# Kernel optimization log

Measured on AMD Instinct MI355X. Metric: run time of the kernel, lower is better.

The kernel has to match this reference:

```python
import jax, jax.numpy as jnp
import numpy as np

N_DOF = 7
WIDTH = 1024
BATCH = 8192
EPS = 1e-5
LSIZE = N_DOF * (N_DOF + 1) // 2   # diag (n) + strictly-lower ((n^2-n)/2)


def _tri_idx(n):
    # order matches LowTri: offset -i chunks, within-chunk j -> entry (j+i, j)
    r, c = [], []
    for i in range(n):
        for j in range(n - i):
            r.append(j + i)
            c.append(j)
    return np.array(r, np.int32), np.array(c, np.int32)

_R, _C = _tri_idx(N_DOF)


def setup_inputs() -> dict:
    key = jax.random.key(0)
    ks = jax.random.split(key, 9)

    def glorot(k, shape):
        std = (2.0 / (shape[0] + shape[1])) ** 0.5
        return (jax.random.normal(k, shape, jnp.float32) * std).astype(jnp.float32)

    lower = LSIZE - N_DOF
    b0 = 0.1
    return {
        "state": jax.random.normal(ks[0], (BATCH, N_DOF), jnp.float32),
        "velocity": jax.random.normal(ks[1], (BATCH, N_DOF), jnp.float32),
        "acceleration": jax.random.normal(ks[2], (BATCH, N_DOF), jnp.float32),
        "W_in": glorot(ks[3], (N_DOF, WIDTH)), "b_in": jnp.full((WIDTH,), b0, jnp.float32),
        "W_h": glorot(ks[4], (WIDTH, WIDTH)), "b_h": jnp.full((WIDTH,), b0, jnp.float32),
        "W_g": glorot(ks[5], (WIDTH, 1)), "b_g": jnp.full((1,), b0, jnp.float32),
        "W_ld": glorot(ks[6], (WIDTH, N_DOF)), "b_ld": jnp.full((N_DOF,), b0, jnp.float32),
        "W_lo": glorot(ks[7], (WIDTH, lower)), "b_lo": jnp.full((lower,), b0, jnp.float32),
    }


def _layer(x, der, W, b, act):
    # a: [B, out]; der: [B, in, n_dof] -> [B, out, n_dof]
    a = x @ W + b
    if act == "relu":
        y = jax.nn.relu(a)
        gp = (a > 0).astype(a.dtype)
    else:  # linear
        y = a
        gp = jnp.ones_like(a)
    # diag(g'(a)) @ W^T @ prev_der  ==  g'(a)[:, :, None] * (W^T @ prev_der)
    new_der = gp[:, :, None] * jnp.einsum("io,bid->bod", W, der)
    return y, new_der


def _forward(state, velocity, acceleration,
             W_in, b_in, W_h, b_h, W_g, b_g, W_ld, b_ld, W_lo, b_lo):
    B = state.shape[0]
    eye = jnp.broadcast_to(jnp.eye(N_DOF, dtype=state.dtype), (B, N_DOF, N_DOF))

    y1, d1 = _layer(state, eye, W_in, b_in, "relu")
    y2, d2 = _layer(y1, d1, W_h, b_h, "relu")
    y3, d3 = _layer(y2, d2, W_h, b_h, "relu")   # original reuses hidden_layer1 twice

    V, derV = _layer(y3, d3, W_g, b_g, "linear")       # derV: [B, 1, n_dof]
    l_diag, der_ld = _layer(y3, d3, W_ld, b_ld, "relu")
    l_low, der_lo = _layer(y3, d3, W_lo, b_lo, "linear")

    l = jnp.concatenate([l_diag, l_low], axis=1)          # [B, LSIZE]
    der_l = jnp.concatenate([der_ld, der_lo], axis=1)     # [B, LSIZE, n_dof]

    def lowtri(v):   # [B, LSIZE] -> [B, n, n]
        return jnp.zeros((B, N_DOF, N_DOF), v.dtype).at[:, _R, _C].set(v)

    def lowtri3d(v):  # [B, n_dof, LSIZE] -> [B, n_dof, n, n]
        return jnp.zeros((B, N_DOF, N_DOF, N_DOF), v.dtype).at[:, :, _R, _C].set(v)

    L = lowtri(l)
    LT = jnp.swapaxes(L, 1, 2)
    M = L @ LT + EPS * jnp.eye(N_DOF, dtype=L.dtype)

    dldt = jnp.einsum("bld,bd->bl", der_l, velocity)
    dLdt = lowtri(dldt)
    dMdt = L @ jnp.swapaxes(dLdt, 1, 2) + dLdt @ LT

    dLdq = lowtri3d(jnp.swapaxes(der_l, 1, 2))            # [B, n_dof, n, n]
    dMdq = dLdq @ LT[:, None] + L[:, None] @ jnp.swapaxes(dLdq, 2, 3)

    dMdt_dq = jnp.einsum("bij,bj->bi", dMdt, velocity)
    quad_dq = jnp.einsum("bi,bkij,bj->bk", velocity, dMdq, velocity)
    C = dMdt_dq - 0.5 * quad_dq
    G = derV[:, 0, :]                                      # squeeze [B,1,n_dof]
    Mddq = jnp.einsum("bij,bj->bi", M, acceleration)
    tau_pred = Mddq + C + G
    return tau_pred, M, C, G


def reference(state, velocity, acceleration,
              W_in, b_in, W_h, b_h, W_g, b_g, W_ld, b_ld, W_lo, b_lo):
    return _forward(state, velocity, acceleration,
                    W_in, b_in, W_h, b_h, W_g, b_g, W_ld, b_ld, W_lo, b_lo)
```

## Files before the change

### kernel.cpp

```cpp
#include <hip/hip_runtime.h>
#include <hip/hip_bf16.h>
#include <hip/hip_fp16.h>

#define WIDTH 1024
#define BATCH 8192

typedef __attribute__((ext_vector_type(8))) short short8;
typedef __attribute__((ext_vector_type(8))) _Float16 half8;
typedef __attribute__((ext_vector_type(4))) float floatx4;

typedef __attribute__((address_space(1))) void gvoid;
typedef __attribute__((address_space(3))) void lvoid;

__device__ __forceinline__ void async_copy16(const void* g, void* l) {
    __builtin_amdgcn_global_load_lds((gvoid*)g, (lvoid*)l, 16, 0, 0);
}

__device__ __forceinline__ void split_store(float v, __hip_bfloat16* hi, __hip_bfloat16* lo, long idx) {
    __hip_bfloat16 h = __float2bfloat16(v);
    hi[idx] = h;
    lo[idx] = __float2bfloat16(v - __bfloat162float(h));
}

__device__ __forceinline__ floatx4 mfma16(short8 a, short8 b, floatx4 c) {
    return __builtin_amdgcn_mfma_f32_16x16x32_f16(
        __builtin_bit_cast(half8, a), __builtin_bit_cast(half8, b), c, 0, 0, 0);
}
__device__ __forceinline__ floatx4 mfmabf(short8 a, short8 b, floatx4 c) {
    return __builtin_amdgcn_mfma_f32_16x16x32_bf16(a, b, c, 0, 0, 0);
}

template<int N> __device__ __forceinline__ void waitv() {
    if constexpr (N == 0)      asm volatile("s_waitcnt vmcnt(0)" ::: "memory");
    else if constexpr (N == 4) asm volatile("s_waitcnt vmcnt(4)" ::: "memory");
    else if constexpr (N == 6) asm volatile("s_waitcnt vmcnt(6)" ::: "memory");
    else if constexpr (N == 8) asm volatile("s_waitcnt vmcnt(8)" ::: "memory");
}

__device__ __forceinline__ int swz_col(int s) {
    return ((s & 3) ^ ((s >> 3) & 3)) << 3;
}

__device__ __forceinline__ void xcd_map(int idx, int nm, int& bm, int& bn) {
    if ((nm & 7) == 0) {
        bm = (idx & 7) | ((idx >> 5) << 3);
        bn = (idx >> 3) & 3;
    } else {
        bm = idx >> 2;
        bn = idx & 3;
    }
}

__global__ __launch_bounds__(256) void transpose_k(
    const float* __restrict__ W,
    __hip_bfloat16* __restrict__ Wthb, __hip_bfloat16* __restrict__ Wtlb,
    __half* __restrict__ Wtf)
{
    __shared__ float t[32][33];
    const int tx = threadIdx.x & 31, ty = threadIdx.x >> 5;
    const int bx = blockIdx.x << 5, by = blockIdx.y << 5;
#pragma unroll
    for (int r = 0; r < 32; r += 8)
        t[ty + r][tx] = W[(long)(by + ty + r) * WIDTH + bx + tx];
    __syncthreads();
#pragma unroll
    for (int r = 0; r < 32; r += 8) {
        const float v = t[tx][ty + r];
        const long idx = (long)(bx + ty + r) * WIDTH + by + tx;
        split_store(v, Wthb, Wtlb, idx);
        Wtf[idx] = __float2half(v);
    }
}

__global__ __launch_bounds__(256) void buildwcat_k(
    const float* __restrict__ W_ld, const float* __restrict__ W_lo,
    const float* __restrict__ W_g,
    __hip_bfloat16* __restrict__ Wchb, __hip_bfloat16* __restrict__ Wclb,
    __half* __restrict__ Wcf)
{
    const int idx = blockIdx.x * 256 + threadIdx.x;
    const int n = idx >> 10, k = idx & 1023;
    float v = 0.f;
    if (n < 7)       v = W_ld[k * 7 + n];
    else if (n < 28) v = W_lo[k * 21 + (n - 7)];
    else if (n == 28) v = W_g[k];
    split_store(v, Wchb, Wclb, idx);
    Wcf[idx] = __float2half(v);
}

__global__ __launch_bounds__(256) void prep_k(
    const float* __restrict__ state,
    const float* __restrict__ W_in,
    const float* __restrict__ b_in,
    __hip_bfloat16* __restrict__ Y1h, __hip_bfloat16* __restrict__ Y1l,
    __half* __restrict__ D1f)
{
    const int b = blockIdx.x;
    const int j0 = threadIdx.x * 4;
    float s[7];
#pragma unroll
    for (int d = 0; d < 7; ++d) s[d] = state[b * 7 + d];
    float a[4];
#pragma unroll
    for (int q = 0; q < 4; ++q) a[q] = b_in[j0 + q];
    float w[7][4];
#pragma unroll
    for (int d = 0; d < 7; ++d)
#pragma unroll
        for (int q = 0; q < 4; ++q) {
            w[d][q] = W_in[d * WIDTH + j0 + q];
            a[q] += s[d] * w[d][q];
        }
    bool gp[4];
#pragma unroll
    for (int q = 0; q < 4; ++q) {
        gp[q] = a[q] > 0.f;
        split_store(gp[q] ? a[q] : 0.f, Y1h, Y1l, (long)b * WIDTH + j0 + q);
    }
    union { unsigned long long u64; unsigned short h[4]; } pk;
#pragma unroll
    for (int d = 0; d < 7; ++d) {
#pragma unroll
        for (int q = 0; q < 4; ++q) {
            __half v = __float2half(gp[q] ? w[d][q] : 0.f);
            pk.h[q] = *reinterpret_cast<unsigned short*>(&v);
        }
        *reinterpret_cast<unsigned long long*>(&D1f[((long)b * 7 + d) * WIDTH + j0]) = pk.u64;
    }
}

__device__ __forceinline__ void st128(const short* src, short* region, int tid, int kbase) {
    async_copy16(src + (long)(tid >> 2) * WIDTH + kbase + swz_col(tid),
                 region + ((tid & 0x1C0) << 3));
}
__device__ __forceinline__ void st256(const short* src, short* region, int tid, int kbase) {
#pragma unroll
    for (int j = 0; j < 2; ++j) {
        const int idx = tid + (j << 9);
        async_copy16(src + (long)(idx >> 2) * WIDTH + kbase + swz_col(idx),
                     region + (((tid & 0x1C0) + (j << 9)) << 3));
    }
}


__device__ __forceinline__ void y_stage(
    short* SM, const short* pAh, const short* pAl,
    const short* pBh, const short* pBl, int c, int tid)
{
    short* buf = SM + (c % 3) * 24576;
    const int kb = c * 32;
    st128(pAh, buf,         tid, kb);
    st256(pBh, buf + 8192,  tid, kb);
    st128(pAl, buf + 4096,  tid, kb);
    st256(pBl, buf + 16384, tid, kb);
}

__device__ __forceinline__ void y_reads(
    const short* SM, int c, int wm, int wn, int r, int kqs,
    short8 (&ah)[4], short8 (&al)[4], short8 (&bh)[4], short8 (&bl)[4])
{
    const short* buf = SM + (c % 3) * 24576;
#pragma unroll
    for (int i = 0; i < 4; ++i) {
        ah[i] = *reinterpret_cast<const short8*>(&buf[(wm * 64 + i * 16 + r) * 32 + kqs]);
        al[i] = *reinterpret_cast<const short8*>(&buf[4096 + (wm * 64 + i * 16 + r) * 32 + kqs]);
    }
#pragma unroll
    for (int j = 0; j < 4; ++j) {
        bh[j] = *reinterpret_cast<const short8*>(&buf[8192 + (wn * 64 + j * 16 + r) * 32 + kqs]);
        bl[j] = *reinterpret_cast<const short8*>(&buf[16384 + (wn * 64 + j * 16 + r) * 32 + kqs]);
    }
}

__device__ __forceinline__ void y8_gemm_body(
    short* SM,
    int bm, int bn, int tid,
    const __hip_bfloat16* Ah_, const __hip_bfloat16* Al_,
    const __hip_bfloat16* Bh_, const __hip_bfloat16* Bl_,
    const float* bias,
    __hip_bfloat16* outh, __hip_bfloat16* outl)
{
    const int lane = tid & 63, wv = tid >> 6;
    const int wm = wv >> 2, wn = wv & 3;
    const int r = lane & 15, r4 = (lane >> 4) << 2;
    const int kqs = (((lane >> 4) ^ ((r >> 1) & 3)) << 3);
    const short* pAh = (const short*)Ah_ + (long)bm * 128 * WIDTH;
    const short* pAl = (const short*)Al_ + (long)bm * 128 * WIDTH;
    const short* pBh = (const short*)Bh_ + (long)bn * 256 * WIDTH;
    const short* pBl = (const short*)Bl_ + (long)bn * 256 * WIDTH;

    floatx4 acc[4][4] = {};
    short8 ahA[4], alA[4], bhA[4], blA[4];
    short8 ahB[4], alB[4], bhB[4], blB[4];

    y_stage(SM, pAh, pAl, pBh, pBl, 0, tid);
    y_stage(SM, pAh, pAl, pBh, pBl, 1, tid);
    y_stage(SM, pAh, pAl, pBh, pBl, 2, tid);
    waitv<6>();
    __builtin_amdgcn_s_barrier();
    y_reads(SM, 0, wm, wn, r, kqs, ahA, alA, bhA, blA);

    auto chunk = [&](short8 (&cah)[4], short8 (&cal)[4], short8 (&cbh)[4], short8 (&cbl)[4],
                     short8 (&nah)[4], short8 (&nal)[4], short8 (&nbh)[4], short8 (&nbl)[4],
                     int c) {
        __builtin_amdgcn_s_barrier();
        if (c + 3 < 32) y_stage(SM, pAh, pAl, pBh, pBl, c + 3, tid);
        if (c + 1 < 32) y_reads(SM, c + 1, wm, wn, r, kqs, nah, nal, nbh, nbl);
        __builtin_amdgcn_s_setprio(1);
#pragma unroll
        for (int i = 0; i < 4; ++i)
#pragma unroll
            for (int j = 0; j < 4; ++j)
                acc[i][j] = mfmabf(cah[i], cbh[j], acc[i][j]);
#pragma unroll
        for (int i = 0; i < 4; ++i)
#pragma unroll
            for (int j = 0; j < 4; ++j)
                acc[i][j] = mfmabf(cal[i], cbh[j], acc[i][j]);
#pragma unroll
        for (int i = 0; i < 4; ++i)
#pragma unroll
            for (int j = 0; j < 4; ++j)
                acc[i][j] = mfmabf(cah[i], cbl[j], acc[i][j]);
        __builtin_amdgcn_s_setprio(0);
        if (c <= 28) waitv<6>();
        else if (c == 29) waitv<0>();
    };

    for (int t2 = 0; t2 < 16; ++t2) {
        chunk(ahA, alA, bhA, blA, ahB, alB, bhB, blB, 2 * t2);
        chunk(ahB, alB, bhB, blB, ahA, alA, bhA, blA, 2 * t2 + 1);
    }

#pragma unroll
    for (int i = 0; i < 4; ++i)
#pragma unroll
        for (int j = 0; j < 4; ++j) {
            const int col = bn * 256 + wn * 64 + j * 16 + r;
#pragma unroll
            for (int rr = 0; rr < 4; ++rr) {
                const int row = bm * 128 + wm * 64 + i * 16 + r4 + rr;
                float v = acc[i][j][rr] + bias[col];
                v = v > 0.f ? v : 0.f;
                split_store(v, outh, outl, (long)row * WIDTH + col);
            }
        }
}

__global__ __launch_bounds__(512, 2) void gemm_y8(
    const __hip_bfloat16* __restrict__ Ah, const __hip_bfloat16* __restrict__ Al,
    const __hip_bfloat16* __restrict__ Bh, const __hip_bfloat16* __restrict__ Bl,
    const float* __restrict__ bias,
    __hip_bfloat16* __restrict__ outh, __hip_bfloat16* __restrict__ outl,
    int ny)
{
    __shared__ __align__(16) short SM[73728];
    int bm, bn;
    xcd_map(blockIdx.x, ny, bm, bn);
    y8_gemm_body(SM, bm, bn, threadIdx.x, Ah, Al, Bh, Bl, bias, outh, outl);
}


__device__ __forceinline__ void stage_chunk_d2(
    short* SMbase, const short* __restrict__ A, const short* __restrict__ B,
    int tau, int creg, int tid)
{
    const short* src = (creg & 1) ? B : A;
    const int kbase = (tau << 6) + ((creg >> 1) << 5);
    short* region = SMbase + ((tau & 1) << 15) + (creg << 13);
    const int wvb = tid & 0x1C0;
#pragma unroll
    for (int j = 0; j < 2; ++j) {
        const int idx = tid + (j << 9);
        async_copy16(src + (long)(idx >> 2) * WIDTH + kbase + swz_col(idx),
                     region + ((long)(wvb + (j << 9)) << 3));
    }
}

__device__ __forceinline__ void d_stage(
    short* SM, const short* A, const short* B, int c, int tid)
{
    stage_chunk_d2(SM, A, B, c >> 1, (c & 1) << 1, tid);
    stage_chunk_d2(SM, A, B, c >> 1, ((c & 1) << 1) | 1, tid);
}

__device__ __forceinline__ void d_reads(
    const short* SM, int c, int wm, int wn, int r, int kqs,
    short8 (&af)[8], short8 (&bf)[4])
{
    const short* Ab = SM + (((c >> 1) & 1) << 15) + ((c & 1) << 14);
    const short* Bb = Ab + 8192;
#pragma unroll
    for (int i = 0; i < 8; ++i)
        af[i] = *reinterpret_cast<const short8*>(&Ab[(wm * 128 + i * 16 + r) * 32 + kqs]);
#pragma unroll
    for (int j = 0; j < 4; ++j)
        bf[j] = *reinterpret_cast<const short8*>(&Bb[(wn * 64 + j * 16 + r) * 32 + kqs]);
}

__device__ __forceinline__ void d_gemm_256(
    short* SM, const short* Abase, const short* Bbase, int tid,
    int wm, int wn, int r, int kqs, floatx4 (&acc)[8][4])
{
    short8 afA[8], bfA[4], afB[8], bfB[4];

    d_stage(SM, Abase, Bbase, 0, tid);
    d_stage(SM, Abase, Bbase, 1, tid);
    d_stage(SM, Abase, Bbase, 2, tid);
    d_stage(SM, Abase, Bbase, 3, tid);
    waitv<8>();
    __builtin_amdgcn_s_barrier();
    d_reads(SM, 0, wm, wn, r, kqs, afA, bfA);

    auto chunk = [&](short8 (&caf)[8], short8 (&cbf)[4],
                     short8 (&naf)[8], short8 (&nbf)[4], int c) {
        __builtin_amdgcn_s_barrier();
        if (c + 4 < 32) d_stage(SM, Abase, Bbase, c + 4, tid);
        if (c + 1 < 32) d_reads(SM, c + 1, wm, wn, r, kqs, naf, nbf);
        __builtin_amdgcn_s_setprio(1);
#pragma unroll
        for (int i = 0; i < 8; ++i)
#pragma unroll
            for (int j = 0; j < 4; ++j)
                acc[i][j] = mfma16(caf[i], cbf[j], acc[i][j]);
        __builtin_amdgcn_s_setprio(0);
        if (c <= 27) waitv<8>();
        else if (c == 28) waitv<4>();
        else if (c == 29) waitv<0>();
    };

    for (int t2 = 0; t2 < 16; ++t2) {
        chunk(afA, bfA, afB, bfB, 2 * t2);
        chunk(afB, bfB, afA, bfA, 2 * t2 + 1);
    }
}

__global__ __launch_bounds__(512, 2) void d2y3_8p(
    const __half* __restrict__ D1,
    const __half* __restrict__ Wtf,
    const __hip_bfloat16* __restrict__ Wthb, const __hip_bfloat16* __restrict__ Wtlb,
    const __hip_bfloat16* __restrict__ Y2h, const __hip_bfloat16* __restrict__ Y2l,
    const float* __restrict__ bias,
    __half* __restrict__ D2out,
    __hip_bfloat16* __restrict__ Y3h, __hip_bfloat16* __restrict__ Y3l,
    int ny128, int nd2)
{
    __shared__ __align__(16) short SM[73728];
    const int tid = threadIdx.x;

    if ((int)blockIdx.x < ny128 * 4) {
        int bm, bn;
        xcd_map(blockIdx.x, ny128, bm, bn);
        y8_gemm_body(SM, bm, bn, tid, Y2h, Y2l, Wthb, Wtlb, bias, Y3h, Y3l);
        return;
    }

    const int lane = tid & 63, wv = tid >> 6;
    const int wm = wv >> 2, wn = wv & 3;
    const int r = lane & 15, r4 = (lane >> 4) << 2;
    const int kqs = (((lane >> 4) ^ ((r >> 1) & 3)) << 3);

    int bm, bn;
    xcd_map(blockIdx.x - ny128 * 4, nd2, bm, bn);

    floatx4 acc[8][4] = {};
    d_gemm_256(SM, (const short*)D1 + (long)bm * 256 * WIDTH,
               (const short*)Wtf + (long)bn * 256 * WIDTH, tid, wm, wn, r, kqs, acc);

#pragma unroll
    for (int i = 0; i < 8; ++i)
#pragma unroll
        for (int j = 0; j < 4; ++j) {
            const int col = bn * 256 + wn * 64 + j * 16 + r;
#pragma unroll
            for (int rr = 0; rr < 4; ++rr) {
                const int row = bm * 256 + wm * 128 + i * 16 + r4 + rr;
                float v = acc[i][j][rr];
                const unsigned brow = (unsigned)row / 7u;
                if (!(__bfloat162float(Y2h[(long)brow * WIDTH + col]) > 0.f)) v = 0.f;
                D2out[(long)row * WIDTH + col] = __float2half(v);
            }
        }
}

__device__ __forceinline__ void heady_half(
    short* SMh, int bm, int tl,
    const __hip_bfloat16* __restrict__ Y3h, const __hip_bfloat16* __restrict__ Y3l,
    const __hip_bfloat16* __restrict__ Wch, const __hip_bfloat16* __restrict__ Wcl,
    float* __restrict__ PY)
{
    short* Ash = SMh;          short* Asl = SMh + 4096;
    short* Bsh = SMh + 8192;   short* Bsl = SMh + 9216;
    const int lane = tl & 63;
    const int wv = tl >> 6;
    const int r = lane & 15, r4 = (lane >> 4) << 2;
    const int kqs = (((lane >> 4) ^ ((r >> 1) & 3)) << 3);
    const int srow = tl >> 2, scol = (tl & 3) << 3;
    const int swc = (((tl & 3) ^ ((srow >> 1) & 3)) << 3);
    const long half = 64l * WIDTH;
    const short* pAh = (const short*)Y3h + (long)(bm * 128 + srow) * WIDTH + swc;
    const short* pAl = (const short*)Y3l + (long)(bm * 128 + srow) * WIDTH + swc;
    const long boff = (long)srow * WIDTH + scol;
    const short* pBh = (const short*)Wch;  const short* pBl = (const short*)Wcl;

    floatx4 acc[2][2] = {};
    for (int kt = 0; kt < WIDTH; kt += 32) {
        short8 gbh, gbl;
        if (tl < 128) {
            gbh = *reinterpret_cast<const short8*>(pBh + boff + kt);
            gbl = *reinterpret_cast<const short8*>(pBl + boff + kt);
        }
        __syncthreads();
        async_copy16(pAh + kt,        Ash + wv * 512);
        async_copy16(pAh + half + kt, Ash + 2048 + wv * 512);
        async_copy16(pAl + kt,        Asl + wv * 512);
        async_copy16(pAl + half + kt, Asl + 2048 + wv * 512);
        if (tl < 128) {
            *reinterpret_cast<short8*>(&Bsh[srow * 32 + swc]) = gbh;
            *reinterpret_cast<short8*>(&Bsl[srow * 32 + swc]) = gbl;
        }
        __syncthreads();
        short8 afh[2], afl[2], bfh[2], bfl[2];
#pragma unroll
        for (int i = 0; i < 2; ++i) {
            const int ar = (wv * 32 + i * 16 + r) * 32 + kqs;
            afh[i] = *reinterpret_cast<const short8*>(&Ash[ar]);
            afl[i] = *reinterpret_cast<const short8*>(&Asl[ar]);
        }
#pragma unroll
        for (int j = 0; j < 2; ++j) {
            const int br = (j * 16 + r) * 32 + kqs;
            bfh[j] = *reinterpret_cast<const short8*>(&Bsh[br]);
            bfl[j] = *reinterpret_cast<const short8*>(&Bsl[br]);
        }
#pragma unroll
        for (int i = 0; i < 2; ++i)
#pragma unroll
            for (int j = 0; j < 2; ++j) {
                acc[i][j] = mfmabf(afh[i], bfh[j], acc[i][j]);
                acc[i][j] = mfmabf(afh[i], bfl[j], acc[i][j]);
                acc[i][j] = mfmabf(afl[i], bfh[j], acc[i][j]);
            }
    }
#pragma unroll
    for (int i = 0; i < 2; ++i)
#pragma unroll
        for (int j = 0; j < 2; ++j)
#pragma unroll
            for (int rr = 0; rr < 4; ++rr) {
                const int row = bm * 128 + wv * 32 + i * 16 + r4 + rr;
                PY[(long)row * 32 + j * 16 + r] = acc[i][j][rr];
            }
}

__global__ __launch_bounds__(512, 2) void d3pd_8p(
    const __half* __restrict__ D2,
    const __half* __restrict__ Wtf,
    const __hip_bfloat16* __restrict__ Y3h, const __hip_bfloat16* __restrict__ Y3l,
    const __half* __restrict__ Wcf,
    const __hip_bfloat16* __restrict__ Wchb, const __hip_bfloat16* __restrict__ Wclb,
    float* __restrict__ PDpart, float* __restrict__ PY,
    int nd2, int Mrows)
{
    __shared__ __align__(16) short SM[65536];
    const int tid = threadIdx.x;

    if ((int)blockIdx.x >= nd2 * 4) {
        const int hd = (blockIdx.x - nd2 * 4) * 2 + (tid >> 8);
        heady_half(SM + (tid >> 8) * 10240, hd, tid & 255, Y3h, Y3l, Wchb, Wclb, PY);
        return;
    }

    const int lane = tid & 63, wv = tid >> 6;
    const int wm = wv >> 2, wn = wv & 3;
    const int r = lane & 15, kq = (lane >> 4) << 3, r4 = (lane >> 4) << 2;
    const int kqs = (((lane >> 4) ^ ((r >> 1) & 3)) << 3);
    int bm, bn;
    xcd_map(blockIdx.x, nd2, bm, bn);

    floatx4 acc[8][4] = {};
    d_gemm_256(SM, (const short*)D2 + (long)bm * 256 * WIDTH,
               (const short*)Wtf + (long)bn * 256 * WIDTH, tid, wm, wn, r, kqs, acc);

    short* T   = SM;
    short* WcH = SM + 34816;

    floatx4 accp[2][2] = {};
#pragma unroll
    for (int h = 0; h < 2; ++h) {
        __syncthreads();
        if ((wn >> 1) == h) {
#pragma unroll
            for (int i = 0; i < 8; ++i)
#pragma unroll
                for (int j = 0; j < 4; ++j) {
                    const int ct = (wn & 1) * 64 + j * 16 + r;
                    const int colg = bn * 256 + h * 128 + ct;
#pragma unroll
                    for (int rr = 0; rr < 4; ++rr) {
                        const int rowl = wm * 128 + i * 16 + r4 + rr;
                        const int rowg = bm * 256 + rowl;
                        float v = acc[i][j][rr];
                        const unsigned brow = (unsigned)rowg / 7u;
                        if (!(__bfloat162float(Y3h[(long)brow * WIDTH + colg]) > 0.f)) v = 0.f;
                        __half hb = __float2half(v);
                        T[rowl * 136 + ct] = *reinterpret_cast<short*>(&hb);
                    }
                }
        }
        {
            const int n = tid >> 4, k8 = (tid & 15) * 8;
            const short* wh = (const short*)Wcf;
            *reinterpret_cast<short8*>(&WcH[n * 136 + k8]) =
                *reinterpret_cast<const short8*>(wh + (long)n * WIDTH + bn * 256 + h * 128 + k8);
        }
        __syncthreads();
#pragma unroll
        for (int kk = 0; kk < 128; kk += 32) {
            short8 af2[2], bh8[2];
#pragma unroll
            for (int i = 0; i < 2; ++i)
                af2[i] = *reinterpret_cast<const short8*>(&T[(wv * 32 + i * 16 + r) * 136 + kk + kq]);
#pragma unroll
            for (int j = 0; j < 2; ++j)
                bh8[j] = *reinterpret_cast<const short8*>(&WcH[(j * 16 + r) * 136 + kk + kq]);
#pragma unroll
            for (int i = 0; i < 2; ++i)
#pragma unroll
                for (int j = 0; j < 2; ++j)
                    accp[i][j] = mfma16(af2[i], bh8[j], accp[i][j]);
        }
    }
#pragma unroll
    for (int i = 0; i < 2; ++i)
#pragma unroll
        for (int j = 0; j < 2; ++j)
#pragma unroll
            for (int rr = 0; rr < 4; ++rr) {
                const int rowg = bm * 256 + wv * 32 + i * 16 + r4 + rr;
                PDpart[((long)bn * Mrows + rowg) * 32 + j * 16 + r] = accp[i][j][rr];
            }
}

__device__ __forceinline__ int midx(int rr, int cc) {
    const int i = rr - cc;
    return i * 7 - (i * (i - 1)) / 2 + cc;
}

__global__ __launch_bounds__(64) void finalize_k(
    const float* __restrict__ PY,
    const float* __restrict__ PDpart,
    const float* __restrict__ vel_g,
    const float* __restrict__ acc_g,
    const float* __restrict__ b_ld,
    const float* __restrict__ b_lo,
    float* __restrict__ out,
    int b0, int Mrows)
{
    __shared__ float lval[28];
    __shared__ int gpv[7];
    __shared__ float derl[29 * 7];
    __shared__ float Lm[49], Mm[49], dLt[49], uu[49];
    __shared__ float wvv[7], pv[7], Cv[7], Gv[7], tauv[7], vl[7], ac[7];

    const int bl = blockIdx.x, tid = threadIdx.x;
    const int b = b0 + bl;
    if (tid < 28) {
        float s = PY[(long)bl * 32 + tid];
        if (tid < 7) {
            s += b_ld[tid];
            gpv[tid] = s > 0.f;
            lval[tid] = s > 0.f ? s : 0.f;
        } else {
            lval[tid] = s + b_lo[tid - 7];
        }
    }
    if (tid >= 28 && tid < 35) {
        vl[tid - 28] = vel_g[b * 7 + tid - 28];
        ac[tid - 28] = acc_g[b * 7 + tid - 28];
    }
    __syncthreads();
    for (int idx = tid; idx < 203; idx += 64) {
        const int m = idx / 7, d = idx % 7;
        float v = 0.f;
#pragma unroll
        for (int p = 0; p < 4; ++p)
            v += PDpart[((long)p * Mrows + bl * 7 + d) * 32 + m];
        if (m < 7 && !gpv[m]) v = 0.f;
        derl[m * 7 + d] = v;
    }
    __syncthreads();
    if (tid < 49) {
        const int rr = tid / 7, cc = tid % 7;
        Lm[tid] = (rr >= cc) ? lval[midx(rr, cc)] : 0.f;
    }
    __syncthreads();
    if (tid < 49) {
        const int rr = tid / 7, cc = tid % 7;
        float s = 0.f;
        for (int k = 0; k < 7; ++k) s += Lm[rr * 7 + k] * Lm[cc * 7 + k];
        if (rr == cc) s += 1e-5f;
        Mm[tid] = s;
        float t = 0.f;
        if (rr >= cc) {
            const int m = midx(rr, cc);
            for (int d = 0; d < 7; ++d) t += derl[m * 7 + d] * vl[d];
        }
        dLt[tid] = t;
        float u = 0.f;
        for (int r2 = cc; r2 < 7; ++r2) u += vl[r2] * derl[midx(r2, cc) * 7 + rr];
        uu[tid] = u;
    } else if (tid >= 49 && tid < 56) {
        const int j = tid - 49;
        float s = 0.f;
        for (int r2 = 0; r2 < 7; ++r2) s += Lm[r2 * 7 + j] * vl[r2];
        wvv[j] = s;
    }
    __syncthreads();
    if (tid < 7) {
        float s = 0.f;
        for (int r2 = 0; r2 < 7; ++r2) s += dLt[r2 * 7 + tid] * vl[r2];
        pv[tid] = s;
    }
    __syncthreads();
    if (tid < 7) {
        float s = 0.f, q = 0.f, md = 0.f;
        for (int c = 0; c < 7; ++c) {
            s += Lm[tid * 7 + c] * pv[c] + dLt[tid * 7 + c] * wvv[c];
            q += uu[tid * 7 + c] * wvv[c];
            md += Mm[tid * 7 + c] * ac[c];
        }
        Cv[tid] = s - q;
        Gv[tid] = derl[28 * 7 + tid];
        tauv[tid] = md + Cv[tid] + Gv[tid];
    }
    __syncthreads();
    if (tid < 49) out[57344 + (long)b * 49 + tid] = Mm[tid];
    if (tid < 7) {
        out[(long)b * 7 + tid] = tauv[tid];
        out[458752 + (long)b * 7 + tid] = Cv[tid];
        out[516096 + (long)b * 7 + tid] = Gv[tid];
    }
}

extern "C" void kernel_launch(void* const* d_in, const int* in_sizes, int n_in,
                              void* d_out, int out_size, void* d_ws, size_t ws_size,
                              hipStream_t stream)
{
    const float* state = (const float*)d_in[0];
    const float* vel   = (const float*)d_in[1];
    const float* accel = (const float*)d_in[2];
    const float* W_in  = (const float*)d_in[3];
    const float* b_in  = (const float*)d_in[4];
    const float* W_h   = (const float*)d_in[5];
    const float* b_h   = (const float*)d_in[6];
    const float* W_g   = (const float*)d_in[7];
    const float* W_ld  = (const float*)d_in[9];
    const float* b_ld  = (const float*)d_in[10];
    const float* W_lo  = (const float*)d_in[11];
    const float* b_lo  = (const float*)d_in[12];
    float* outp = (float*)d_out;

    char* ws = (char*)d_ws;
    __hip_bfloat16* Wthb = (__hip_bfloat16*)ws; ws += (size_t)WIDTH * WIDTH * 2;
    __hip_bfloat16* Wtlb = (__hip_bfloat16*)ws; ws += (size_t)WIDTH * WIDTH * 2;
    __half*         Wtf  = (__half*)ws;         ws += (size_t)WIDTH * WIDTH * 2;
    __hip_bfloat16* Wchb = (__hip_bfloat16*)ws; ws += 32 * WIDTH * 2;
    __hip_bfloat16* Wclb = (__hip_bfloat16*)ws; ws += 32 * WIDTH * 2;
    __half*         Wcf  = (__half*)ws;         ws += 32 * WIDTH * 2;
    const size_t fixed = (size_t)(ws - (char*)d_ws);

    int CH = 256;
    for (int cand = 8192; cand >= 256; cand >>= 1) {
        size_t need = fixed + (size_t)cand * 36992;
        if (need <= ws_size) { CH = cand; break; }
    }
    const int NCH = BATCH / CH;

    const size_t YB = (size_t)CH * WIDTH * 2;
    const size_t DB = (size_t)CH * 7 * WIDTH * 2;
    __hip_bfloat16* Yah = (__hip_bfloat16*)ws; ws += YB;
    __hip_bfloat16* Yal = (__hip_bfloat16*)ws; ws += YB;
    __hip_bfloat16* Ybh = (__hip_bfloat16*)ws; ws += YB;
    __hip_bfloat16* Ybl = (__hip_bfloat16*)ws; ws += YB;
    __half* Daf = (__half*)ws; ws += DB;
    __half* Dbf = (__half*)ws; ws += DB;
    float* PY = (float*)ws; ws += (size_t)CH * 32 * 4;
    float* PDpart = (float*)Daf;

    const int Mrows = CH * 7;
    const int nd2 = Mrows / 256;
    const int ny128 = CH / 128;

    transpose_k<<<dim3(32, 32), dim3(256), 0, stream>>>(W_h, Wthb, Wtlb, Wtf);
    buildwcat_k<<<dim3(128), dim3(256), 0, stream>>>(W_ld, W_lo, W_g, Wchb, Wclb, Wcf);

    for (int c = 0; c < NCH; ++c) {
        prep_k<<<dim3(CH), dim3(256), 0, stream>>>(state + (size_t)c * CH * 7, W_in, b_in,
                                                   Yah, Yal, Daf);
        gemm_y8<<<dim3(ny128 * 4), dim3(512), 0, stream>>>(
            Yah, Yal, Wthb, Wtlb, b_h, Ybh, Ybl, ny128);
        d2y3_8p<<<dim3((ny128 + nd2) * 4), dim3(512), 0, stream>>>(
            Daf, Wtf, Wthb, Wtlb, Ybh, Ybl, b_h, Dbf, Yah, Yal, ny128, nd2);
        d3pd_8p<<<dim3(nd2 * 4 + ny128 / 2), dim3(512), 0, stream>>>(
            Dbf, Wtf, Yah, Yal, Wcf, Wchb, Wclb, PDpart, PY, nd2, Mrows);
        finalize_k<<<dim3(CH), dim3(64), 0, stream>>>(PY, PDpart, vel, accel, b_ld, b_lo,
                                                      outp, c * CH, Mrows);
    }
    (void)in_sizes; (void)n_in; (void)out_size;
}
```

Before: 553.5 us.

## Split fused D2/Y3 kernel and shrink derivative GEMM tiles to 128x256 with 256 threads

```diff
diff --git a/kernel.cpp b/kernel.cpp
--- a/kernel.cpp
+++ b/kernel.cpp
@@ -31,10 +31,9 @@
 }
 
 template<int N> __device__ __forceinline__ void waitv() {
-    if constexpr (N == 0)      asm volatile("s_waitcnt vmcnt(0)" ::: "memory");
-    else if constexpr (N == 4) asm volatile("s_waitcnt vmcnt(4)" ::: "memory");
-    else if constexpr (N == 6) asm volatile("s_waitcnt vmcnt(6)" ::: "memory");
-    else if constexpr (N == 8) asm volatile("s_waitcnt vmcnt(8)" ::: "memory");
+    if constexpr (N == 0)       asm volatile("s_waitcnt vmcnt(0)" ::: "memory");
+    else if constexpr (N == 6)  asm volatile("s_waitcnt vmcnt(6)" ::: "memory");
+    else if constexpr (N == 8)  asm volatile("s_waitcnt vmcnt(8)" ::: "memory");
 }
 
 __device__ __forceinline__ int swz_col(int s) {
@@ -142,7 +141,6 @@
     }
 }
 
-
 __device__ __forceinline__ void y_stage(
     short* SM, const short* pAh, const short* pAl,
     const short* pBh, const short* pBl, int c, int tid)
@@ -261,62 +259,64 @@
 }
 
 
-__device__ __forceinline__ void stage_chunk_d2(
-    short* SMbase, const short* __restrict__ A, const short* __restrict__ B,
-    int tau, int creg, int tid)
-{
-    const short* src = (creg & 1) ? B : A;
-    const int kbase = (tau << 6) + ((creg >> 1) << 5);
-    short* region = SMbase + ((tau & 1) << 15) + (creg << 13);
-    const int wvb = tid & 0x1C0;
+__device__ __forceinline__ void stA4(const short* src, short* region, int tid, int kb) {
+    const int wvb = tid & 0xC0;
 #pragma unroll
     for (int j = 0; j < 2; ++j) {
-        const int idx = tid + (j << 9);
-        async_copy16(src + (long)(idx >> 2) * WIDTH + kbase + swz_col(idx),
-                     region + ((long)(wvb + (j << 9)) << 3));
-    }
-}
-
-__device__ __forceinline__ void d_stage(
+        const int idx = tid + (j << 8);
+        async_copy16(src + (long)(idx >> 2) * WIDTH + kb + swz_col(idx),
+                     region + (((j << 8) + wvb) << 3));
+    }
+}
+__device__ __forceinline__ void stB4(const short* src, short* region, int tid, int kb) {
+    const int wvb = tid & 0xC0;
+#pragma unroll
+    for (int j = 0; j < 4; ++j) {
+        const int idx = tid + (j << 8);
+        async_copy16(src + (long)(idx >> 2) * WIDTH + kb + swz_col(idx),
+                     region + (((j << 8) + wvb) << 3));
+    }
+}
+
+__device__ __forceinline__ void d4_stage(
     short* SM, const short* A, const short* B, int c, int tid)
 {
-    stage_chunk_d2(SM, A, B, c >> 1, (c & 1) << 1, tid);
-    stage_chunk_d2(SM, A, B, c >> 1, ((c & 1) << 1) | 1, tid);
-}
-
-__device__ __forceinline__ void d_reads(
-    const short* SM, int c, int wm, int wn, int r, int kqs,
+    short* slot = SM + (c % 3) * 12288;
+    stA4(A, slot,        tid, c * 32);
+    stB4(B, slot + 4096, tid, c * 32);
+}
+
+__device__ __forceinline__ void d4_reads(
+    const short* SM, int c, int wn, int r, int kqs,
     short8 (&af)[8], short8 (&bf)[4])
 {
-    const short* Ab = SM + (((c >> 1) & 1) << 15) + ((c & 1) << 14);
-    const short* Bb = Ab + 8192;
+    const short* buf = SM + (c % 3) * 12288;
 #pragma unroll
     for (int i = 0; i < 8; ++i)
-        af[i] = *reinterpret_cast<const short8*>(&Ab[(wm * 128 + i * 16 + r) * 32 + kqs]);
+        af[i] = *reinterpret_cast<const short8*>(&buf[(i * 16 + r) * 32 + kqs]);
 #pragma unroll
     for (int j = 0; j < 4; ++j)
-        bf[j] = *reinterpret_cast<const short8*>(&Bb[(wn * 64 + j * 16 + r) * 32 + kqs]);
-}
-
-__device__ __forceinline__ void d_gemm_256(
+        bf[j] = *reinterpret_cast<const short8*>(&buf[4096 + (wn * 64 + j * 16 + r) * 32 + kqs]);
+}
+
+__device__ __forceinline__ void d4_gemm(
     short* SM, const short* Abase, const short* Bbase, int tid,
-    int wm, int wn, int r, int kqs, floatx4 (&acc)[8][4])
+    int wn, int r, int kqs, floatx4 (&acc)[8][4])
 {
     short8 afA[8], bfA[4], afB[8], bfB[4];
 
-    d_stage(SM, Abase, Bbase, 0, tid);
-    d_stage(SM, Abase, Bbase, 1, tid);
-    d_stage(SM, Abase, Bbase, 2, tid);
-    d_stage(SM, Abase, Bbase, 3, tid);
-    waitv<8>();
+    d4_stage(SM, Abase, Bbase, 0, tid);
+    d4_stage(SM, Abase, Bbase, 1, tid);
+    d4_stage(SM, Abase, Bbase, 2, tid);
+    waitv<6>();
     __builtin_amdgcn_s_barrier();
-    d_reads(SM, 0, wm, wn, r, kqs, afA, bfA);
+    d4_reads(SM, 0, wn, r, kqs, afA, bfA);
 
     auto chunk = [&](short8 (&caf)[8], short8 (&cbf)[4],
                      short8 (&naf)[8], short8 (&nbf)[4], int c) {
         __builtin_amdgcn_s_barrier();
-        if (c + 4 < 32) d_stage(SM, Abase, Bbase, c + 4, tid);
-        if (c + 1 < 32) d_reads(SM, c + 1, wm, wn, r, kqs, naf, nbf);
+        if (c + 1 < 32) d4_reads(SM, c + 1, wn, r, kqs, naf, nbf);
+        if (c + 3 < 32) d4_stage(SM, Abase, Bbase, c + 3, tid);
         __builtin_amdgcn_s_setprio(1);
 #pragma unroll
         for (int i = 0; i < 8; ++i)
@@ -324,8 +324,7 @@
             for (int j = 0; j < 4; ++j)
                 acc[i][j] = mfma16(caf[i], cbf[j], acc[i][j]);
         __builtin_amdgcn_s_setprio(0);
-        if (c <= 27) waitv<8>();
-        else if (c == 28) waitv<4>();
+        if (c <= 28) waitv<6>();
         else if (c == 29) waitv<0>();
     };
 
@@ -335,37 +334,24 @@
     }
 }
 
-__global__ __launch_bounds__(512, 2) void d2y3_8p(
+__global__ __launch_bounds__(256, 2) void gemm_d2(
     const __half* __restrict__ D1,
     const __half* __restrict__ Wtf,
-    const __hip_bfloat16* __restrict__ Wthb, const __hip_bfloat16* __restrict__ Wtlb,
-    const __hip_bfloat16* __restrict__ Y2h, const __hip_bfloat16* __restrict__ Y2l,
-    const float* __restrict__ bias,
+    const __hip_bfloat16* __restrict__ Y2h,
     __half* __restrict__ D2out,
-    __hip_bfloat16* __restrict__ Y3h, __hip_bfloat16* __restrict__ Y3l,
-    int ny128, int nd2)
-{
-    __shared__ __align__(16) short SM[73728];
+    int nm)
+{
+    __shared__ __align__(16) short SM[36864];
     const int tid = threadIdx.x;
-
-    if ((int)blockIdx.x < ny128 * 4) {
-        int bm, bn;
-        xcd_map(blockIdx.x, ny128, bm, bn);
-        y8_gemm_body(SM, bm, bn, tid, Y2h, Y2l, Wthb, Wtlb, bias, Y3h, Y3l);
-        return;
-    }
-
-    const int lane = tid & 63, wv = tid >> 6;
-    const int wm = wv >> 2, wn = wv & 3;
+    const int lane = tid & 63, wn = tid >> 6;
     const int r = lane & 15, r4 = (lane >> 4) << 2;
     const int kqs = (((lane >> 4) ^ ((r >> 1) & 3)) << 3);
-
     int bm, bn;
-    xcd_map(blockIdx.x - ny128 * 4, nd2, bm, bn);
+    xcd_map(blockIdx.x, nm, bm, bn);
 
     floatx4 acc[8][4] = {};
-    d_gemm_256(SM, (const short*)D1 + (long)bm * 256 * WIDTH,
-               (const short*)Wtf + (long)bn * 256 * WIDTH, tid, wm, wn, r, kqs, acc);
+    d4_gemm(SM, (const short*)D1 + (long)bm * 128 * WIDTH,
+            (const short*)Wtf + (long)bn * 256 * WIDTH, tid, wn, r, kqs, acc);
 
 #pragma unroll
     for (int i = 0; i < 8; ++i)
@@ -374,7 +360,7 @@
             const int col = bn * 256 + wn * 64 + j * 16 + r;
 #pragma unroll
             for (int rr = 0; rr < 4; ++rr) {
-                const int row = bm * 256 + wm * 128 + i * 16 + r4 + rr;
+                const int row = bm * 128 + i * 16 + r4 + rr;
                 float v = acc[i][j][rr];
                 const unsigned brow = (unsigned)row / 7u;
                 if (!(__bfloat162float(Y2h[(long)brow * WIDTH + col]) > 0.f)) v = 0.f;
@@ -453,37 +439,35 @@
             }
 }
 
-__global__ __launch_bounds__(512, 2) void d3pd_8p(
+__global__ __launch_bounds__(256, 2) void d3pd_k(
     const __half* __restrict__ D2,
     const __half* __restrict__ Wtf,
     const __hip_bfloat16* __restrict__ Y3h, const __hip_bfloat16* __restrict__ Y3l,
     const __half* __restrict__ Wcf,
     const __hip_bfloat16* __restrict__ Wchb, const __hip_bfloat16* __restrict__ Wclb,
     float* __restrict__ PDpart, float* __restrict__ PY,
-    int nd2, int Mrows)
-{
-    __shared__ __align__(16) short SM[65536];
+    int nm, int Mrows)
+{
+    __shared__ __align__(16) short SM[36864];
     const int tid = threadIdx.x;
 
-    if ((int)blockIdx.x >= nd2 * 4) {
-        const int hd = (blockIdx.x - nd2 * 4) * 2 + (tid >> 8);
-        heady_half(SM + (tid >> 8) * 10240, hd, tid & 255, Y3h, Y3l, Wchb, Wclb, PY);
+    if ((int)blockIdx.x >= nm * 4) {
+        heady_half(SM, blockIdx.x - nm * 4, tid, Y3h, Y3l, Wchb, Wclb, PY);
         return;
     }
 
-    const int lane = tid & 63, wv = tid >> 6;
-    const int wm = wv >> 2, wn = wv & 3;
+    const int lane = tid & 63, wn = tid >> 6;
     const int r = lane & 15, kq = (lane >> 4) << 3, r4 = (lane >> 4) << 2;
     const int kqs = (((lane >> 4) ^ ((r >> 1) & 3)) << 3);
     int bm, bn;
-    xcd_map(blockIdx.x, nd2, bm, bn);
+    xcd_map(blockIdx.x, nm, bm, bn);
 
     floatx4 acc[8][4] = {};
-    d_gemm_256(SM, (const short*)D2 + (long)bm * 256 * WIDTH,
-               (const short*)Wtf + (long)bn * 256 * WIDTH, tid, wm, wn, r, kqs, acc);
+    d4_gemm(SM, (const short*)D2 + (long)bm * 128 * WIDTH,
+            (const short*)Wtf + (long)bn * 256 * WIDTH, tid, wn, r, kqs, acc);
 
     short* T   = SM;
-    short* WcH = SM + 34816;
+    short* WcH = SM + 17408;
 
     floatx4 accp[2][2] = {};
 #pragma unroll
@@ -498,8 +482,8 @@
                     const int colg = bn * 256 + h * 128 + ct;
 #pragma unroll
                     for (int rr = 0; rr < 4; ++rr) {
-                        const int rowl = wm * 128 + i * 16 + r4 + rr;
-                        const int rowg = bm * 256 + rowl;
+                        const int rowl = i * 16 + r4 + rr;
+                        const int rowg = bm * 128 + rowl;
                         float v = acc[i][j][rr];
                         const unsigned brow = (unsigned)rowg / 7u;
                         if (!(__bfloat162float(Y3h[(long)brow * WIDTH + colg]) > 0.f)) v = 0.f;
@@ -513,6 +497,8 @@
             const short* wh = (const short*)Wcf;
             *reinterpret_cast<short8*>(&WcH[n * 136 + k8]) =
                 *reinterpret_cast<const short8*>(wh + (long)n * WIDTH + bn * 256 + h * 128 + k8);
+            *reinterpret_cast<short8*>(&WcH[(n + 16) * 136 + k8]) =
+                *reinterpret_cast<const short8*>(wh + (long)(n + 16) * WIDTH + bn * 256 + h * 128 + k8);
         }
         __syncthreads();
 #pragma unroll
@@ -520,7 +506,7 @@
             short8 af2[2], bh8[2];
 #pragma unroll
             for (int i = 0; i < 2; ++i)
-                af2[i] = *reinterpret_cast<const short8*>(&T[(wv * 32 + i * 16 + r) * 136 + kk + kq]);
+                af2[i] = *reinterpret_cast<const short8*>(&T[(wn * 32 + i * 16 + r) * 136 + kk + kq]);
 #pragma unroll
             for (int j = 0; j < 2; ++j)
                 bh8[j] = *reinterpret_cast<const short8*>(&WcH[(j * 16 + r) * 136 + kk + kq]);
@@ -537,7 +523,7 @@
         for (int j = 0; j < 2; ++j)
 #pragma unroll
             for (int rr = 0; rr < 4; ++rr) {
-                const int rowg = bm * 256 + wv * 32 + i * 16 + r4 + rr;
+                const int rowg = bm * 128 + wn * 32 + i * 16 + r4 + rr;
                 PDpart[((long)bn * Mrows + rowg) * 32 + j * 16 + r] = accp[i][j][rr];
             }
 }
@@ -689,7 +675,7 @@
     float* PDpart = (float*)Daf;
 
     const int Mrows = CH * 7;
-    const int nd2 = Mrows / 256;
+    const int nm128 = Mrows / 128;
     const int ny128 = CH / 128;
 
     transpose_k<<<dim3(32, 32), dim3(256), 0, stream>>>(W_h, Wthb, Wtlb, Wtf);
@@ -700,10 +686,12 @@
                                                    Yah, Yal, Daf);
         gemm_y8<<<dim3(ny128 * 4), dim3(512), 0, stream>>>(
             Yah, Yal, Wthb, Wtlb, b_h, Ybh, Ybl, ny128);
-        d2y3_8p<<<dim3((ny128 + nd2) * 4), dim3(512), 0, stream>>>(
-            Daf, Wtf, Wthb, Wtlb, Ybh, Ybl, b_h, Dbf, Yah, Yal, ny128, nd2);
-        d3pd_8p<<<dim3(nd2 * 4 + ny128 / 2), dim3(512), 0, stream>>>(
-            Dbf, Wtf, Yah, Yal, Wcf, Wchb, Wclb, PDpart, PY, nd2, Mrows);
+        gemm_y8<<<dim3(ny128 * 4), dim3(512), 0, stream>>>(
+            Ybh, Ybl, Wthb, Wtlb, b_h, Yah, Yal, ny128);
+        gemm_d2<<<dim3(nm128 * 4), dim3(256), 0, stream>>>(
+            Daf, Wtf, Ybh, Dbf, nm128);
+        d3pd_k<<<dim3(nm128 * 4 + ny128), dim3(256), 0, stream>>>(
+            Dbf, Wtf, Yah, Yal, Wcf, Wchb, Wclb, PDpart, PY, nm128, Mrows);
         finalize_k<<<dim3(CH), dim3(64), 0, stream>>>(PY, PDpart, vel, accel, b_ld, b_lo,
                                                       outp, c * CH, Mrows);
     }
```

Result: slower. 615.3 us (+11.2%).

## Rewrite d3 derivative GEMM as 256-thread blocks with 128x128 warp tiles

Applied to the files above, without the earlier changes.

```diff
diff --git a/kernel.cpp b/kernel.cpp
--- a/kernel.cpp
+++ b/kernel.cpp
@@ -31,10 +31,10 @@
 }
 
 template<int N> __device__ __forceinline__ void waitv() {
-    if constexpr (N == 0)      asm volatile("s_waitcnt vmcnt(0)" ::: "memory");
-    else if constexpr (N == 4) asm volatile("s_waitcnt vmcnt(4)" ::: "memory");
-    else if constexpr (N == 6) asm volatile("s_waitcnt vmcnt(6)" ::: "memory");
-    else if constexpr (N == 8) asm volatile("s_waitcnt vmcnt(8)" ::: "memory");
+    if constexpr (N == 0)       asm volatile("s_waitcnt vmcnt(0)" ::: "memory");
+    else if constexpr (N == 4)  asm volatile("s_waitcnt vmcnt(4)" ::: "memory");
+    else if constexpr (N == 6)  asm volatile("s_waitcnt vmcnt(6)" ::: "memory");
+    else if constexpr (N == 8)  asm volatile("s_waitcnt vmcnt(8)" ::: "memory");
 }
 
 __device__ __forceinline__ int swz_col(int s) {
@@ -142,7 +142,6 @@
     }
 }
 
-
 __device__ __forceinline__ void y_stage(
     short* SM, const short* pAh, const short* pAl,
     const short* pBh, const short* pBl, int c, int tid)
@@ -259,7 +258,6 @@
     xcd_map(blockIdx.x, ny, bm, bn);
     y8_gemm_body(SM, bm, bn, threadIdx.x, Ah, Al, Bh, Bl, bias, outh, outl);
 }
-
 
 __device__ __forceinline__ void stage_chunk_d2(
     short* SMbase, const short* __restrict__ A, const short* __restrict__ B,
@@ -381,6 +379,71 @@
                 D2out[(long)row * WIDTH + col] = __float2half(v);
             }
         }
+}
+
+
+__device__ __forceinline__ void stR(const short* src, short* region, int tid, int kb) {
+    const int wvb = tid & 0xC0;
+#pragma unroll
+    for (int k = 0; k < 4; ++k) {
+        const int idx = tid + (k << 8);
+        async_copy16(src + (long)(idx >> 2) * WIDTH + kb + swz_col(idx),
+                     region + (((k << 8) + wvb) << 3));
+    }
+}
+
+__device__ __forceinline__ void d128_stage(short* SM, const short* A, const short* B, int c, int tid) {
+    short* slot = SM + (c % 3) * 16384;
+    stR(A, slot,        tid, c * 32);
+    stR(B, slot + 8192, tid, c * 32);
+}
+
+__device__ __forceinline__ void d128_reads(
+    const short* SM, int c, int wm, int wn, int r, int kqs,
+    short8 (&af)[8], short8 (&bf)[8])
+{
+    const short* slot = SM + (c % 3) * 16384;
+#pragma unroll
+    for (int i = 0; i < 8; ++i)
+        af[i] = *reinterpret_cast<const short8*>(&slot[(wm * 128 + i * 16 + r) * 32 + kqs]);
+#pragma unroll
+    for (int j = 0; j < 8; ++j)
+        bf[j] = *reinterpret_cast<const short8*>(&slot[8192 + (wn * 128 + j * 16 + r) * 32 + kqs]);
+}
+
+__device__ __forceinline__ void d128_gemm(
+    short* SM, const short* Abase, const short* Bbase, int tid,
+    int wm, int wn, int r, int kqs, floatx4 (&acc)[8][8])
+{
+    short8 afA[8], bfA[8], afB[8], bfB[8];
+
+    d128_stage(SM, Abase, Bbase, 0, tid);
+    d128_stage(SM, Abase, Bbase, 1, tid);
+    d128_stage(SM, Abase, Bbase, 2, tid);
+    waitv<8>();
+    __builtin_amdgcn_s_barrier();
+    d128_reads(SM, 0, wm, wn, r, kqs, afA, bfA);
+
+    auto chunk = [&](short8 (&caf)[8], short8 (&cbf)[8],
+                     short8 (&naf)[8], short8 (&nbf)[8], int c) {
+        __builtin_amdgcn_s_barrier();
+        if (c + 1 < 32) d128_reads(SM, c + 1, wm, wn, r, kqs, naf, nbf);
+        if (c + 3 < 32) d128_stage(SM, Abase, Bbase, c + 3, tid);
+        __builtin_amdgcn_s_setprio(1);
+#pragma unroll
+        for (int i = 0; i < 8; ++i)
+#pragma unroll
+            for (int j = 0; j < 8; ++j)
+                acc[i][j] = mfma16(caf[i], cbf[j], acc[i][j]);
+        __builtin_amdgcn_s_setprio(0);
+        if (c <= 28) waitv<8>();
+        else if (c == 29) waitv<0>();
+    };
+
+    for (int t2 = 0; t2 < 16; ++t2) {
+        chunk(afA, bfA, afB, bfB, 2 * t2);
+        chunk(afB, bfB, afA, bfA, 2 * t2 + 1);
+    }
 }
 
 __device__ __forceinline__ void heady_half(
@@ -453,48 +516,47 @@
             }
 }
 
-__global__ __launch_bounds__(512, 2) void d3pd_8p(
+__global__ __launch_bounds__(256, 1) void d3pd128(
     const __half* __restrict__ D2,
     const __half* __restrict__ Wtf,
     const __hip_bfloat16* __restrict__ Y3h, const __hip_bfloat16* __restrict__ Y3l,
     const __half* __restrict__ Wcf,
     const __hip_bfloat16* __restrict__ Wchb, const __hip_bfloat16* __restrict__ Wclb,
     float* __restrict__ PDpart, float* __restrict__ PY,
-    int nd2, int Mrows)
-{
-    __shared__ __align__(16) short SM[65536];
+    int nm, int Mrows)
+{
+    __shared__ __align__(16) short SM[49152];
     const int tid = threadIdx.x;
 
-    if ((int)blockIdx.x >= nd2 * 4) {
-        const int hd = (blockIdx.x - nd2 * 4) * 2 + (tid >> 8);
-        heady_half(SM + (tid >> 8) * 10240, hd, tid & 255, Y3h, Y3l, Wchb, Wclb, PY);
+    if ((int)blockIdx.x >= nm * 4) {
+        heady_half(SM, blockIdx.x - nm * 4, tid, Y3h, Y3l, Wchb, Wclb, PY);
         return;
     }
 
     const int lane = tid & 63, wv = tid >> 6;
-    const int wm = wv >> 2, wn = wv & 3;
+    const int wm = wv >> 1, wn = wv & 1;
     const int r = lane & 15, kq = (lane >> 4) << 3, r4 = (lane >> 4) << 2;
     const int kqs = (((lane >> 4) ^ ((r >> 1) & 3)) << 3);
     int bm, bn;
-    xcd_map(blockIdx.x, nd2, bm, bn);
-
-    floatx4 acc[8][4] = {};
-    d_gemm_256(SM, (const short*)D2 + (long)bm * 256 * WIDTH,
-               (const short*)Wtf + (long)bn * 256 * WIDTH, tid, wm, wn, r, kqs, acc);
+    xcd_map(blockIdx.x, nm, bm, bn);
+
+    floatx4 acc[8][8] = {};
+    d128_gemm(SM, (const short*)D2 + (long)bm * 256 * WIDTH,
+              (const short*)Wtf + (long)bn * 256 * WIDTH, tid, wm, wn, r, kqs, acc);
 
     short* T   = SM;
     short* WcH = SM + 34816;
 
-    floatx4 accp[2][2] = {};
+    floatx4 accp[4][2] = {};
 #pragma unroll
     for (int h = 0; h < 2; ++h) {
         __syncthreads();
-        if ((wn >> 1) == h) {
+        if (wn == h) {
 #pragma unroll
             for (int i = 0; i < 8; ++i)
 #pragma unroll
-                for (int j = 0; j < 4; ++j) {
-                    const int ct = (wn & 1) * 64 + j * 16 + r;
+                for (int j = 0; j < 8; ++j) {
+                    const int ct = j * 16 + r;
                     const int colg = bn * 256 + h * 128 + ct;
 #pragma unroll
                     for (int rr = 0; rr < 4; ++rr) {
@@ -513,31 +575,33 @@
             const short* wh = (const short*)Wcf;
             *reinterpret_cast<short8*>(&WcH[n * 136 + k8]) =
                 *reinterpret_cast<const short8*>(wh + (long)n * WIDTH + bn * 256 + h * 128 + k8);
+            *reinterpret_cast<short8*>(&WcH[(n + 16) * 136 + k8]) =
+                *reinterpret_cast<const short8*>(wh + (long)(n + 16) * WIDTH + bn * 256 + h * 128 + k8);
         }
         __syncthreads();
 #pragma unroll
         for (int kk = 0; kk < 128; kk += 32) {
-            short8 af2[2], bh8[2];
-#pragma unroll
-            for (int i = 0; i < 2; ++i)
-                af2[i] = *reinterpret_cast<const short8*>(&T[(wv * 32 + i * 16 + r) * 136 + kk + kq]);
+            short8 af2[4], bh8[2];
+#pragma unroll
+            for (int i = 0; i < 4; ++i)
+                af2[i] = *reinterpret_cast<const short8*>(&T[(wv * 64 + i * 16 + r) * 136 + kk + kq]);
 #pragma unroll
             for (int j = 0; j < 2; ++j)
                 bh8[j] = *reinterpret_cast<const short8*>(&WcH[(j * 16 + r) * 136 + kk + kq]);
 #pragma unroll
-            for (int i = 0; i < 2; ++i)
+            for (int i = 0; i < 4; ++i)
 #pragma unroll
                 for (int j = 0; j < 2; ++j)
                     accp[i][j] = mfma16(af2[i], bh8[j], accp[i][j]);
         }
     }
 #pragma unroll
-    for (int i = 0; i < 2; ++i)
+    for (int i = 0; i < 4; ++i)
 #pragma unroll
         for (int j = 0; j < 2; ++j)
 #pragma unroll
             for (int rr = 0; rr < 4; ++rr) {
-                const int rowg = bm * 256 + wv * 32 + i * 16 + r4 + rr;
+                const int rowg = bm * 256 + wv * 64 + i * 16 + r4 + rr;
                 PDpart[((long)bn * Mrows + rowg) * 32 + j * 16 + r] = accp[i][j][rr];
             }
 }
@@ -702,7 +766,7 @@
             Yah, Yal, Wthb, Wtlb, b_h, Ybh, Ybl, ny128);
         d2y3_8p<<<dim3((ny128 + nd2) * 4), dim3(512), 0, stream>>>(
             Daf, Wtf, Wthb, Wtlb, Ybh, Ybl, b_h, Dbf, Yah, Yal, ny128, nd2);
-        d3pd_8p<<<dim3(nd2 * 4 + ny128 / 2), dim3(512), 0, stream>>>(
+        d3pd128<<<dim3(nd2 * 4 + ny128), dim3(256), 0, stream>>>(
             Dbf, Wtf, Yah, Yal, Wcf, Wchb, Wclb, PDpart, PY, nd2, Mrows);
         finalize_k<<<dim3(CH), dim3(64), 0, stream>>>(PY, PDpart, vel, accel, b_ld, b_lo,
                                                       outp, c * CH, Mrows);
```

Result: slower. 718.2 us (+29.7%).
